# Kernel optimization log

Hardware: AMD Instinct MI355X
Metric: run time of the kernel (lower is better)

## Reference

```python
import jax, jax.numpy as jnp
import numpy as np

D = 512      # model_size
NH = 8       # num_heads
HD = D // NH # head_dim = 64
T = 2048     # seq len (qlen == klen == pos len)
B = 2        # batch

# flattened Bayesian parameter layout (matches flatten_list order in the module)
_SHAPES = [(3 * D, D), (D, D), (D, D), (3 * D,), (D,), (D,), (NH, HD), (NH, HD)]
_N = sum(int(np.prod(s)) for s in _SHAPES)  # 1,314,304


def _unflatten(w):
    out, i = [], 0
    for s in _SHAPES:
        n = int(np.prod(s))
        out.append(w[i:i + n].reshape(s))
        i += n
    return out


def _rel_shift(x):
    # Transformer-XL relative shift: x is [qlen, klen, B, NH]
    q, k, b, n = x.shape
    x = jnp.pad(x, ((0, 0), (1, 0), (0, 0), (0, 0)))  # zero col at front of klen axis
    x = x.reshape(k + 1, q, b, n)[1:]
    return x.reshape(q, k, b, n)


def setup_inputs() -> dict:
    key = jax.random.key(0)
    k1, k2, k3, k4, k5 = jax.random.split(key, 5)
    inp = jax.random.normal(k1, (T, B, D), dtype=jnp.float32)
    pos = jax.random.normal(k2, (T, 1, D), dtype=jnp.float32)
    std = np.sqrt(2.0 / (D + D))
    mu = jax.random.normal(k3, (_N,), dtype=jnp.float32) * std
    rho = -5.0 + 0.1 * jax.random.normal(k4, (_N,), dtype=jnp.float32)
    eps = jax.random.normal(k5, (_N,), dtype=jnp.float32)
    attn_mask = jnp.triu(jnp.ones((T, T), dtype=bool), 1)  # True = masked (future)
    return {"input": inp, "pos": pos, "attn_mask": attn_mask,
            "mu": mu, "rho": rho, "eps": eps}


def reference(input, pos, attn_mask, mu, rho, eps):
    # Gaussian reparameterized weight sample: w = mu + softplus(rho) * eps
    w = mu + jax.nn.softplus(rho) * eps
    (in_w, out_w, pos_w, in_b, out_b, pos_b, r_w_bias, r_r_bias) = _unflatten(w)

    # input projection -> q, k, v : [T, B, NH, HD]
    qkv = input @ in_w.T + in_b                      # [T, B, 3D]
    q, k, v = jnp.split(qkv, 3, axis=-1)
    q = q.reshape(T, B, NH, HD)
    k = k.reshape(T, B, NH, HD)
    v = v.reshape(T, B, NH, HD)

    # relative position projection: [R, NH, HD]
    r = (pos[:, 0, :] @ pos_w.T + pos_b).reshape(-1, NH, HD)

    # content score (AC) and position score (BD) with rel-shift
    AC = jnp.einsum('ibnd,jbnd->ijbn', q + r_w_bias, k)
    BD = _rel_shift(jnp.einsum('ibnd,jnd->ijbn', q + r_r_bias, r))

    scale = np.float32(1.0 / np.sqrt(HD))
    score = (AC + BD) * scale                        # [T, T, B, NH]
    score = jnp.where(attn_mask[:, :, None, None],
                      jnp.finfo(score.dtype).min, score)
    probs = jax.nn.softmax(score, axis=1)

    attn_vec = jnp.einsum('ijbn,jbnd->ibnd', probs, v).reshape(T, B, D)
    return attn_vec @ out_w.T + out_b                # [T, B, D]
```

## Files before the change

kernel.cpp:

```cpp
#include <hip/hip_runtime.h>


typedef float f32x4 __attribute__((ext_vector_type(4)));
typedef short bf16x8 __attribute__((ext_vector_type(8)));

#define NW 1314304
#define OFF_INB  1310720
#define OFF_INW  0
#define OFF_OUTW 786432
#define OFF_POSW 1048576
#define BB_IN  0
#define BB_OUT 1536
#define BB_POS 2048
#define BB_RW  2560
#define BB_RR  3072

#define L2E 1.44269504088896340736f

__device__ __forceinline__ unsigned short f2bf(float x) {
  unsigned u = __builtin_bit_cast(unsigned, x);
  u += 0x7fffu + ((u >> 16) & 1u);
  return (unsigned short)(u >> 16);
}
__device__ __forceinline__ float bf2f(unsigned short s) {
  return __builtin_bit_cast(float, ((unsigned)s) << 16);
}
__device__ __forceinline__ unsigned pk2(float lo, float hi) {
  return (unsigned)f2bf(lo) | ((unsigned)f2bf(hi) << 16);
}

__global__ void prep_kernel(const float* __restrict__ mu, const float* __restrict__ rho,
                            const float* __restrict__ eps,
                            const float* __restrict__ input, const float* __restrict__ pos,
                            unsigned short* __restrict__ Wh, float* __restrict__ Bf,
                            unsigned short* __restrict__ inH, unsigned short* __restrict__ posH) {
  const int bx = blockIdx.x;
  if (bx < 1284) {
    int i = (bx * 256 + threadIdx.x) * 4;
    if (i < NW) {
      float4 m = *(const float4*)&mu[i];
      float4 r = *(const float4*)&rho[i];
      float4 e = *(const float4*)&eps[i];
      float w0 = m.x + ((r.x > 20.f) ? r.x : log1pf(expf(r.x))) * e.x;
      float w1 = m.y + ((r.y > 20.f) ? r.y : log1pf(expf(r.y))) * e.y;
      float w2 = m.z + ((r.z > 20.f) ? r.z : log1pf(expf(r.z))) * e.z;
      float w3 = m.w + ((r.w > 20.f) ? r.w : log1pf(expf(r.w))) * e.w;
      union { unsigned short s[4]; uint2 u; } p;
      p.s[0] = f2bf(w0); p.s[1] = f2bf(w1); p.s[2] = f2bf(w2); p.s[3] = f2bf(w3);
      *(uint2*)&Wh[i] = p.u;
      if (i >= OFF_INB) {
        float4 b; b.x = w0; b.y = w1; b.z = w2; b.w = w3;
        *(float4*)&Bf[i - OFF_INB] = b;
      }
    }
  } else if (bx < 3332) {
    int i = ((bx - 1284) * 256 + threadIdx.x) * 4;
    float4 v = *(const float4*)&input[i];
    union { unsigned short s[4]; uint2 u; } p;
    p.s[0] = f2bf(v.x); p.s[1] = f2bf(v.y); p.s[2] = f2bf(v.z); p.s[3] = f2bf(v.w);
    *(uint2*)&inH[i] = p.u;
  } else {
    int i = ((bx - 3332) * 256 + threadIdx.x) * 4;
    float4 v = *(const float4*)&pos[i];
    union { unsigned short s[4]; uint2 u; } p;
    p.s[0] = f2bf(v.x); p.s[1] = f2bf(v.y); p.s[2] = f2bf(v.z); p.s[3] = f2bf(v.w);
    *(uint2*)&posH[i] = p.u;
  }
}

__device__ __forceinline__ void gemm_loop(const unsigned short* __restrict__ A,
                                          const unsigned short* __restrict__ B,
                                          unsigned short* As, unsigned short* Bs,
                                          f32x4 (&acc)[4]) {
  const int tid = threadIdx.x;
  const int wv = tid >> 6, lane = tid & 63, g = lane >> 4, cc = lane & 15;
  const int row = tid >> 2, q4 = tid & 3;
  const unsigned short* Ap = A + (size_t)row * 512 + 16 * q4;
  const unsigned short* Bp = B + (size_t)row * 512 + 16 * q4;

  *(uint4*)&As[row * 72 + 16 * q4]     = *(const uint4*)Ap;
  *(uint4*)&As[row * 72 + 16 * q4 + 8] = *(const uint4*)(Ap + 8);
  *(uint4*)&Bs[row * 72 + 16 * q4]     = *(const uint4*)Bp;
  *(uint4*)&Bs[row * 72 + 16 * q4 + 8] = *(const uint4*)(Bp + 8);
  __syncthreads();

  for (int it = 0; it < 8; it++) {
    uint4 a0, a1, b0, b1;
    const bool pf = (it < 7);
    if (pf) {
      const unsigned short* An = Ap + 64 * (it + 1);
      const unsigned short* Bn = Bp + 64 * (it + 1);
      a0 = *(const uint4*)An; a1 = *(const uint4*)(An + 8);
      b0 = *(const uint4*)Bn; b1 = *(const uint4*)(Bn + 8);
    }
    __builtin_amdgcn_s_setprio(1);
#pragma unroll
    for (int ks = 0; ks < 2; ks++) {
      bf16x8 af = *(const bf16x8*)&As[(16 * wv + cc) * 72 + 32 * ks + 8 * g];
#pragma unroll
      for (int fn = 0; fn < 4; fn++) {
        bf16x8 bf = *(const bf16x8*)&Bs[(16 * fn + cc) * 72 + 32 * ks + 8 * g];
        acc[fn] = __builtin_amdgcn_mfma_f32_16x16x32_bf16(af, bf, acc[fn], 0, 0, 0);
      }
    }
    __builtin_amdgcn_s_setprio(0);
    __syncthreads();
    if (pf) {
      *(uint4*)&As[row * 72 + 16 * q4]     = a0;
      *(uint4*)&As[row * 72 + 16 * q4 + 8] = a1;
      *(uint4*)&Bs[row * 72 + 16 * q4]     = b0;
      *(uint4*)&Bs[row * 72 + 16 * q4 + 8] = b1;
    }
    __syncthreads();
  }
}

__global__ __launch_bounds__(256, 2)
void gemm01_kernel(const unsigned short* __restrict__ inH, const unsigned short* __restrict__ posH,
                   const unsigned short* __restrict__ Wh, const float* __restrict__ Bf,
                   unsigned short* __restrict__ qrw, unsigned short* __restrict__ qrr,
                   unsigned short* __restrict__ kbuf, unsigned short* __restrict__ vT,
                   unsigned short* __restrict__ rbuf) {
  __shared__ __align__(16) unsigned short As[64 * 72];
  __shared__ __align__(16) unsigned short Bs[64 * 72];
  const int bx = blockIdx.x;
  const int tid = threadIdx.x;
  const int wv = tid >> 6, lane = tid & 63, g = lane >> 4, cc = lane & 15;

  const bool isR = (bx >= 1536);
  int m0, n0;
  const unsigned short *A, *W;
  if (!isR) {
    m0 = (bx & 63) << 6; n0 = (bx >> 6) << 6;
    A = inH + (size_t)m0 * 512;  W = Wh + OFF_INW + (size_t)n0 * 512;
  } else {
    const int t = bx - 1536;
    m0 = (t & 31) << 6; n0 = (t >> 5) << 6;
    A = posH + (size_t)m0 * 512; W = Wh + OFF_POSW + (size_t)n0 * 512;
  }

  f32x4 acc[4];
#pragma unroll
  for (int i = 0; i < 4; i++) { acc[i][0] = 0.f; acc[i][1] = 0.f; acc[i][2] = 0.f; acc[i][3] = 0.f; }
  gemm_loop(A, W, As, Bs, acc);

  const int nh2 = (n0 >> 6) & 7;
  const int sec = isR ? 3 : (n0 >> 9);

  if (sec == 0) {
#pragma unroll
    for (int fn = 0; fn < 4; fn++) {
      const int col = n0 + 16 * fn + cc;
      const float b0 = Bf[BB_IN + col];
      const float brw = Bf[BB_RW + col], brr = Bf[BB_RR + col];
#pragma unroll
      for (int r = 0; r < 4; r++) {
        const int ml = 16 * wv + 4 * g + r;
        As[ml * 72 + 16 * fn + cc] = f2bf((acc[fn][r] + b0 + brw) * 0.125f);
        Bs[ml * 72 + 16 * fn + cc] = f2bf((acc[fn][r] + b0 + brr) * 0.125f);
      }
    }
    __syncthreads();
    const int t0 = m0 >> 1;
#pragma unroll
    for (int pass = 0; pass < 2; pass++) {
      const int ch = tid + pass * 256;
      const int bb2 = ch >> 8, tl = (ch >> 3) & 31, hc = ch & 7;
      const int ml = 2 * tl + bb2;
      uint4 v1 = *(const uint4*)&As[ml * 72 + 8 * hc];
      uint4 v2 = *(const uint4*)&Bs[ml * 72 + 8 * hc];
      const size_t dst = ((size_t)(bb2 * 8 + nh2) * 2048 + t0 + tl) * 64 + 8 * hc;
      *(uint4*)&qrw[dst] = v1;
      *(uint4*)&qrr[dst] = v2;
    }
  } else if (sec == 1) {
#pragma unroll
    for (int fn = 0; fn < 4; fn++) {
      const int col = n0 + 16 * fn + cc;
      const float b0 = Bf[BB_IN + col];
#pragma unroll
      for (int r = 0; r < 4; r++)
        As[(16 * wv + 4 * g + r) * 72 + 16 * fn + cc] = f2bf(acc[fn][r] + b0);
    }
    __syncthreads();
    const int t0 = m0 >> 1;
#pragma unroll
    for (int pass = 0; pass < 2; pass++) {
      const int ch = tid + pass * 256;
      const int bb2 = ch >> 8, tl = (ch >> 3) & 31, hc = ch & 7;
      const int ml = 2 * tl + bb2;
      uint4 v1 = *(const uint4*)&As[ml * 72 + 8 * hc];
      *(uint4*)&kbuf[((size_t)(bb2 * 8 + nh2) * 2048 + t0 + tl) * 64 + 8 * hc] = v1;
    }
  } else if (sec == 2) {
#pragma unroll
    for (int fn = 0; fn < 4; fn++) {
      const int col = n0 + 16 * fn + cc;
#pragma unroll
      for (int r = 0; r < 4; r++)
        As[(16 * wv + 4 * g + r) * 72 + 16 * fn + cc] = f2bf(acc[fn][r] + Bf[BB_IN + col]);
    }
    __syncthreads();
#pragma unroll
    for (int cpass = 0; cpass < 2; cpass++) {
      const int ch = tid + cpass * 256;
      const int ncol = ch >> 3, bb2 = (ch >> 2) & 1, jc = ch & 3;
      union { unsigned short s[8]; uint4 u; } pk;
#pragma unroll
      for (int jj = 0; jj < 8; jj++)
        pk.s[jj] = As[(2 * (8 * jc + jj) + bb2) * 72 + ncol];
      *(uint4*)&vT[((size_t)(bb2 * 8 + nh2) * 64 + ncol) * 2048 + (m0 >> 1) + 8 * jc] = pk.u;
    }
  } else {
#pragma unroll
    for (int fn = 0; fn < 4; fn++) {
      const int col = n0 + 16 * fn + cc;
      const float b0 = Bf[BB_POS + col];
#pragma unroll
      for (int r = 0; r < 4; r++)
        As[(16 * wv + 4 * g + r) * 72 + 16 * fn + cc] = f2bf(acc[fn][r] + b0);
    }
    __syncthreads();
#pragma unroll
    for (int pass = 0; pass < 2; pass++) {
      const int ch = tid + pass * 256;
      const int ml = ch >> 3, hc = ch & 7;
      uint4 v1 = *(const uint4*)&As[ml * 72 + 8 * hc];
      *(uint4*)&rbuf[((size_t)nh2 * 2048 + m0 + ml) * 64 + 8 * hc] = v1;
    }
  }
}

__global__ __launch_bounds__(256, 2)
void gemmO_kernel(const unsigned short* __restrict__ av, const unsigned short* __restrict__ W,
                  const float* __restrict__ Bf, float* __restrict__ outp) {
  __shared__ __align__(16) unsigned short As[64 * 72];
  __shared__ __align__(16) unsigned short Bs[64 * 72];
  const int bx = blockIdx.x;
  const int tid = threadIdx.x;
  const int wv = tid >> 6, lane = tid & 63, g = lane >> 4, cc = lane & 15;
  const int m0 = (bx & 63) << 6, n0 = (bx >> 6) << 6;

  f32x4 acc[4];
#pragma unroll
  for (int i = 0; i < 4; i++) { acc[i][0] = 0.f; acc[i][1] = 0.f; acc[i][2] = 0.f; acc[i][3] = 0.f; }
  gemm_loop(av + (size_t)m0 * 512, W + (size_t)n0 * 512, As, Bs, acc);

#pragma unroll
  for (int fn = 0; fn < 4; fn++) {
    const int col = n0 + 16 * fn + cc;
#pragma unroll
    for (int r = 0; r < 4; r++) {
      const int mrow = m0 + 16 * wv + 4 * g + r;
      outp[(size_t)mrow * 512 + col] = acc[fn][r] + Bf[BB_OUT + col];
    }
  }
}

__global__ __launch_bounds__(256, 3)
void attn_kernel(const unsigned short* __restrict__ qrw, const unsigned short* __restrict__ qrr,
                 const unsigned short* __restrict__ kb, const unsigned short* __restrict__ vt,
                 const unsigned short* __restrict__ rb, unsigned short* __restrict__ av,
                 unsigned short* __restrict__ pO, float* __restrict__ pStats)
{
  __shared__ __align__(16) unsigned short Ks[64 * 72];
  __shared__ __align__(16) unsigned short Vs[64 * 72];
  __shared__ __align__(16) unsigned short Rs[128 * 72];
  __shared__ __align__(16) unsigned short GPs[4 * 16 * 84];

  const int tid = threadIdx.x;
  const int wv = tid >> 6, lane = tid & 63, g = lane >> 4, cc = lane & 15;
  const int bx = (int)blockIdx.x;
  const int bn = bx & 15;
  const int sid = 79 - (bx >> 4);
  int qt, s, ns;
  if (sid < 8)       { qt = sid;                s = 0;           ns = 1; }
  else if (sid < 24) { qt = 8 + ((sid - 8) >> 1); s = (sid - 8) & 1; ns = 2; }
  else if (sid < 48) { const int t = sid - 24; const int q3 = t / 3; qt = 16 + q3; s = t - 3 * q3; ns = 3; }
  else               { const int t = sid - 48; qt = 24 + (t >> 2); s = t & 3; ns = 4; }
  const int kt0 = s * 8;
  const int kt1 = (kt0 + 8 < qt + 1) ? (kt0 + 8) : (qt + 1);

  const int nh = bn & 7, bb = bn >> 3;
  const int i0 = qt * 64;
  const int i0g = i0 + wv * 16;
  const int w0base = 1984 - i0;

  const size_t qko = (size_t)bn * 2048 * 64;
  const size_t ro = (size_t)nh * 2048 * 64;

  bf16x8 qw[2], qr[2];
#pragma unroll
  for (int ks = 0; ks < 2; ks++) {
    qw[ks] = *(const bf16x8*)&qrw[qko + (size_t)(i0g + cc) * 64 + 32 * ks + 8 * g];
    qr[ks] = *(const bf16x8*)&qrr[qko + (size_t)(i0g + cc) * 64 + 32 * ks + 8 * g];
  }

  float m_run = -3.0e38f, l_run = 0.f;
  f32x4 o[4];
#pragma unroll
  for (int i = 0; i < 4; i++) { o[i][0] = 0.f; o[i][1] = 0.f; o[i][2] = 0.f; o[i][3] = 0.f; }

  const int srow = tid >> 2, sq = tid & 3;
  const int rrow = tid >> 1, rhalf = tid & 1;
  unsigned short* Gw = &GPs[wv * 1344];
  const int rbase = 48 - 16 * wv;

  {
    const unsigned short* kp = &kb[qko + (size_t)(kt0 * 64 + srow) * 64 + 16 * sq];
    *(uint4*)&Ks[srow * 72 + 16 * sq]     = *(const uint4*)kp;
    *(uint4*)&Ks[srow * 72 + 16 * sq + 8] = *(const uint4*)(kp + 8);
    const unsigned short* vp = &vt[qko + (size_t)srow * 2048 + kt0 * 64 + 16 * sq];
    *(uint4*)&Vs[srow * 72 + 16 * sq]     = *(const uint4*)vp;
    *(uint4*)&Vs[srow * 72 + 16 * sq + 8] = *(const uint4*)(vp + 8);
    const int u0 = w0base + kt0 * 64 + rrow;
    const int uc0 = u0 > 2047 ? 2047 : u0;
    const unsigned short* rp = &rb[ro + (size_t)uc0 * 64 + 32 * rhalf];
    unsigned short* rd = &Rs[(u0 & 127) * 72 + 32 * rhalf];
    *(uint4*)rd        = *(const uint4*)rp;
    *(uint4*)(rd + 8)  = *(const uint4*)(rp + 8);
    *(uint4*)(rd + 16) = *(const uint4*)(rp + 16);
    *(uint4*)(rd + 24) = *(const uint4*)(rp + 24);
  }
  __syncthreads();

  for (int kt = kt0; kt < kt1; kt++) {
    const int j0 = kt * 64;
    const int w0k = w0base + j0;
    const bool pf = (kt + 1 < kt1);

    uint4 ka0, ka1, va0, va1, ra0, ra1;
    int rslot = 0;
    if (pf) {
      const unsigned short* kp = &kb[qko + (size_t)(j0 + 64 + srow) * 64 + 16 * sq];
      ka0 = *(const uint4*)kp; ka1 = *(const uint4*)(kp + 8);
      const unsigned short* vp = &vt[qko + (size_t)srow * 2048 + j0 + 64 + 16 * sq];
      va0 = *(const uint4*)vp; va1 = *(const uint4*)(vp + 8);
      const int unew = w0k + 128 + (tid >> 2);
      rslot = unew & 127;
      const int uc = unew > 2047 ? 2047 : unew;
      const unsigned short* rp = &rb[ro + (size_t)uc * 64 + 16 * sq];
      ra0 = *(const uint4*)rp; ra1 = *(const uint4*)(rp + 8);
    }

    f32x4 st[4];
#pragma unroll
    for (int i = 0; i < 4; i++) { st[i][0] = 0.f; st[i][1] = 0.f; st[i][2] = 0.f; st[i][3] = 0.f; }
    __builtin_amdgcn_s_setprio(1);
#pragma unroll
    for (int ks = 0; ks < 2; ks++) {
#pragma unroll
      for (int fm = 0; fm < 4; fm++) {
        bf16x8 ka = *(const bf16x8*)&Ks[(16 * fm + cc) * 72 + 32 * ks + 8 * g];
        st[fm] = __builtin_amdgcn_mfma_f32_16x16x32_bf16(ka, qw[ks], st[fm], 0, 0, 0);
      }
    }
    f32x4 gt[5];
#pragma unroll
    for (int i = 0; i < 5; i++) { gt[i][0] = 0.f; gt[i][1] = 0.f; gt[i][2] = 0.f; gt[i][3] = 0.f; }
    const int rr0 = w0k + rbase + cc;
#pragma unroll
    for (int ks = 0; ks < 2; ks++) {
#pragma unroll
      for (int fm = 0; fm < 5; fm++) {
        const int rrw = (rr0 + 16 * fm) & 127;
        bf16x8 ra = *(const bf16x8*)&Rs[rrw * 72 + 32 * ks + 8 * g];
        gt[fm] = __builtin_amdgcn_mfma_f32_16x16x32_bf16(ra, qr[ks], gt[fm], 0, 0, 0);
      }
    }
    __builtin_amdgcn_s_setprio(0);

#pragma unroll
    for (int fm = 0; fm < 5; fm++) {
      uint2 w;
      w.x = pk2(gt[fm][0], gt[fm][1]);
      w.y = pk2(gt[fm][2], gt[fm][3]);
      *(uint2*)&Gw[cc * 84 + 16 * fm + 4 * g] = w;
    }

    float p[4][4];
    float tm = -3.0e38f;
    const bool diag = (kt == qt);
    const int c00 = 15 - cc + 4 * g;
#pragma unroll
    for (int fm = 0; fm < 4; fm++) {
      const int c0 = c00 + 16 * fm;
      const int e0 = c0 & ~1;
      const unsigned short* gp = &Gw[cc * 84 + e0];
      unsigned d0 = *(const unsigned*)gp;
      unsigned d1 = *(const unsigned*)(gp + 2);
      unsigned d2 = *(const unsigned*)(gp + 4);
      unsigned lo01, lo23;
      if (c0 & 1) { lo01 = (d0 >> 16) | (d1 << 16); lo23 = (d1 >> 16) | (d2 << 16); }
      else        { lo01 = d0; lo23 = d1; }
      float bd0 = bf2f((unsigned short)(lo01 & 0xffffu));
      float bd1 = bf2f((unsigned short)(lo01 >> 16));
      float bd2 = bf2f((unsigned short)(lo23 & 0xffffu));
      float bd3 = bf2f((unsigned short)(lo23 >> 16));
      float sv0 = st[fm][0] + bd0;
      float sv1 = st[fm][1] + bd1;
      float sv2 = st[fm][2] + bd2;
      float sv3 = st[fm][3] + bd3;
      if (diag) {
        const int jj = 16 * fm + 4 * g;
        const int lim = cc + 16 * wv;
        if (jj + 0 > lim) sv0 = -3.0e38f;
        if (jj + 1 > lim) sv1 = -3.0e38f;
        if (jj + 2 > lim) sv2 = -3.0e38f;
        if (jj + 3 > lim) sv3 = -3.0e38f;
      }
      p[fm][0] = sv0; p[fm][1] = sv1; p[fm][2] = sv2; p[fm][3] = sv3;
      tm = fmaxf(tm, fmaxf(fmaxf(sv0, sv1), fmaxf(sv2, sv3)));
    }
    tm = fmaxf(tm, __shfl_xor(tm, 16));
    tm = fmaxf(tm, __shfl_xor(tm, 32));
    const float m_new = fmaxf(m_run, tm);
    const float sc = exp2f((m_run - m_new) * L2E);
    float ps = 0.f;
#pragma unroll
    for (int fm = 0; fm < 4; fm++)
#pragma unroll
      for (int r = 0; r < 4; r++) {
        float pv = exp2f((p[fm][r] - m_new) * L2E);
        p[fm][r] = pv;
        ps += pv;
      }
    ps += __shfl_xor(ps, 16);
    ps += __shfl_xor(ps, 32);
    l_run = l_run * sc + ps;
    m_run = m_new;

    float scr[4];
#pragma unroll
    for (int r = 0; r < 4; r++) scr[r] = __shfl(sc, 4 * g + r);
#pragma unroll
    for (int fn = 0; fn < 4; fn++)
#pragma unroll
      for (int r = 0; r < 4; r++) o[fn][r] *= scr[r];

#pragma unroll
    for (int fm = 0; fm < 4; fm++) {
      uint2 w;
      w.x = pk2(p[fm][0], p[fm][1]);
      w.y = pk2(p[fm][2], p[fm][3]);
      *(uint2*)&Gw[cc * 72 + 16 * fm + 4 * g] = w;
    }
    bf16x8 pa[2];
#pragma unroll
    for (int ks = 0; ks < 2; ks++)
      pa[ks] = *(const bf16x8*)&Gw[cc * 72 + 32 * ks + 8 * g];

    __builtin_amdgcn_s_setprio(1);
#pragma unroll
    for (int ks = 0; ks < 2; ks++) {
#pragma unroll
      for (int fn = 0; fn < 4; fn++) {
        bf16x8 vb = *(const bf16x8*)&Vs[(16 * fn + cc) * 72 + 32 * ks + 8 * g];
        o[fn] = __builtin_amdgcn_mfma_f32_16x16x32_bf16(pa[ks], vb, o[fn], 0, 0, 0);
      }
    }
    __builtin_amdgcn_s_setprio(0);

    __syncthreads();
    if (pf) {
      *(uint4*)&Ks[srow * 72 + 16 * sq]     = ka0;
      *(uint4*)&Ks[srow * 72 + 16 * sq + 8] = ka1;
      *(uint4*)&Vs[srow * 72 + 16 * sq]     = va0;
      *(uint4*)&Vs[srow * 72 + 16 * sq + 8] = va1;
      unsigned short* rd = &Rs[rslot * 72 + 16 * sq];
      *(uint4*)rd       = ra0;
      *(uint4*)(rd + 8) = ra1;
    }
    __syncthreads();
  }

  if (ns == 1) {
    const float inv = 1.0f / l_run;
    float invr[4];
#pragma unroll
    for (int r = 0; r < 4; r++) invr[r] = __shfl(inv, 4 * g + r);
#pragma unroll
    for (int fn = 0; fn < 4; fn++) {
      const int hd = 16 * fn + cc;
#pragma unroll
      for (int r = 0; r < 4; r++) {
        const int irow = i0g + 4 * g + r;
        av[((size_t)(irow * 2 + bb) * 8 + nh) * 64 + hd] = f2bf(o[fn][r] * invr[r]);
      }
    }
  } else {
    const size_t slot = (size_t)(bn * 80 + sid);
#pragma unroll
    for (int fn = 0; fn < 4; fn++) {
      const int hd = 16 * fn + cc;
#pragma unroll
      for (int r = 0; r < 4; r++)
        pO[slot * 4096 + (16 * wv + 4 * g + r) * 64 + hd] = f2bf(o[fn][r]);
    }
    if (g == 0) {
      pStats[slot * 128 + (16 * wv + cc) * 2]     = m_run;
      pStats[slot * 128 + (16 * wv + cc) * 2 + 1] = l_run;
    }
  }
}

__global__ __launch_bounds__(256)
void combine_kernel(const unsigned short* __restrict__ pO, const float* __restrict__ pStats,
                    unsigned short* __restrict__ av) {
  const int bxx = (int)blockIdx.x;
  const int bn = bxx & 15, qt = 8 + (bxx >> 4);
  const int nh = bn & 7, bb = bn >> 3;
  const int ns = (qt >> 3) + 1;
  const int sid0 = (qt < 16) ? (8 + (qt - 8) * 2)
                 : (qt < 24) ? (24 + (qt - 16) * 3)
                             : (48 + (qt - 24) * 4);
  const int tid = threadIdx.x;
  const int ql = tid >> 2, hq = tid & 3;
  const size_t sb = (size_t)(bn * 80 + sid0);

  float M = -3.0e38f;
  for (int i = 0; i < ns; i++)
    M = fmaxf(M, pStats[(sb + i) * 128 + ql * 2]);

  float L = 0.f;
  float accv[16];
#pragma unroll
  for (int j = 0; j < 16; j++) accv[j] = 0.f;
  for (int i = 0; i < ns; i++) {
    const float mi = pStats[(sb + i) * 128 + ql * 2];
    const float li = pStats[(sb + i) * 128 + ql * 2 + 1];
    const float w = exp2f((mi - M) * L2E);
    L += w * li;
    union { uint4 u; unsigned short s[8]; } c0, c1;
    const unsigned short* src = &pO[(sb + i) * 4096 + ql * 64 + 16 * hq];
    c0.u = *(const uint4*)src;
    c1.u = *(const uint4*)(src + 8);
#pragma unroll
    for (int j = 0; j < 8; j++) accv[j]     += w * bf2f(c0.s[j]);
#pragma unroll
    for (int j = 0; j < 8; j++) accv[8 + j] += w * bf2f(c1.s[j]);
  }
  const float inv = 1.0f / L;
  union { uint4 u; unsigned short s[8]; } o0, o1;
#pragma unroll
  for (int j = 0; j < 8; j++) o0.s[j] = f2bf(accv[j] * inv);
#pragma unroll
  for (int j = 0; j < 8; j++) o1.s[j] = f2bf(accv[8 + j] * inv);
  const int q = qt * 64 + ql;
  unsigned short* dst = &av[((size_t)(q * 2 + bb) * 8 + nh) * 64 + 16 * hq];
  *(uint4*)dst       = o0.u;
  *(uint4*)(dst + 8) = o1.u;
}

extern "C" void kernel_launch(void* const* d_in, const int* in_sizes, int n_in,
                              void* d_out, int out_size, void* d_ws, size_t ws_size,
                              hipStream_t stream) {
  const float* input = (const float*)d_in[0];
  const float* pos   = (const float*)d_in[1];
  const float* mu  = (const float*)d_in[3];
  const float* rho = (const float*)d_in[4];
  const float* eps = (const float*)d_in[5];
  float* out = (float*)d_out;

  char* ws = (char*)d_ws;
  unsigned short* Wh   = (unsigned short*)ws;
  float*          Bf   = (float*)(ws + 2628608);
  unsigned short* inH  = (unsigned short*)(ws + 2642944);
  unsigned short* posH = (unsigned short*)(ws + 6837248);
  unsigned short* qrw  = (unsigned short*)(ws + 8934400);
  unsigned short* qrr  = (unsigned short*)(ws + 13128704);
  unsigned short* kbuf = (unsigned short*)(ws + 17323008);
  unsigned short* vT   = (unsigned short*)(ws + 21517312);
  unsigned short* rbuf = (unsigned short*)(ws + 25711616);
  unsigned short* pO   = (unsigned short*)(ws + 27808768);
  float*          pSt  = (float*)(ws + 38294528);
  unsigned short* av   = inH;

  prep_kernel<<<dim3(4356), dim3(256), 0, stream>>>(mu, rho, eps, input, pos, Wh, Bf, inH, posH);
  gemm01_kernel<<<dim3(1792), dim3(256), 0, stream>>>(inH, posH, Wh, Bf, qrw, qrr, kbuf, vT, rbuf);
  attn_kernel<<<dim3(1280), dim3(256), 0, stream>>>(qrw, qrr, kbuf, vT, rbuf, av, pO, pSt);
  combine_kernel<<<dim3(384), dim3(256), 0, stream>>>(pO, pSt, av);
  gemmO_kernel<<<dim3(512), dim3(256), 0, stream>>>(av, Wh + OFF_OUTW, Bf, out);
}
```

Measured before the change: 171.5 us.

## Enlarge projection GEMM tiles to 128x128 and defer softmax rescaling in attention

Both projection GEMMs (QKV/pos and output) now use 128x128 block tiles with a 2x2 wave layout and 4x4 MFMA accumulators per wave. This raises operand reuse per LDS load and cuts the block count, but it also lowers grid parallelism (128 blocks for gemmO on a large GPU) and raises register pressure. Separately, the attention kernel skips the running-max update and the output rescale when every lane's tile max exceeds the current max by at most 8. That leaves exponentials up to e^8 in fp32, which stays numerically safe.

```diff
diff --git a/kernel.cpp b/kernel.cpp
--- a/kernel.cpp
+++ b/kernel.cpp
@@ -68,48 +68,61 @@
   }
 }
 
-__device__ __forceinline__ void gemm_loop(const unsigned short* __restrict__ A,
-                                          const unsigned short* __restrict__ B,
-                                          unsigned short* As, unsigned short* Bs,
-                                          f32x4 (&acc)[4]) {
+__device__ __forceinline__ void gemm128_loop(const unsigned short* __restrict__ A,
+                                             const unsigned short* __restrict__ B,
+                                             unsigned short* As, unsigned short* Bs,
+                                             f32x4 (&acc)[4][4]) {
   const int tid = threadIdx.x;
   const int wv = tid >> 6, lane = tid & 63, g = lane >> 4, cc = lane & 15;
-  const int row = tid >> 2, q4 = tid & 3;
-  const unsigned short* Ap = A + (size_t)row * 512 + 16 * q4;
-  const unsigned short* Bp = B + (size_t)row * 512 + 16 * q4;
-
-  *(uint4*)&As[row * 72 + 16 * q4]     = *(const uint4*)Ap;
-  *(uint4*)&As[row * 72 + 16 * q4 + 8] = *(const uint4*)(Ap + 8);
-  *(uint4*)&Bs[row * 72 + 16 * q4]     = *(const uint4*)Bp;
-  *(uint4*)&Bs[row * 72 + 16 * q4 + 8] = *(const uint4*)(Bp + 8);
+  const int wr = wv >> 1, wc = wv & 1;
+  const int row = tid >> 1, half = tid & 1;
+  const unsigned short* Ap = A + (size_t)row * 512 + 32 * half;
+  const unsigned short* Bp = B + (size_t)row * 512 + 32 * half;
+  const int lb = row * 72 + 32 * half;
+
+#pragma unroll
+  for (int j = 0; j < 4; j++) {
+    *(uint4*)&As[lb + 8 * j] = *(const uint4*)(Ap + 8 * j);
+    *(uint4*)&Bs[lb + 8 * j] = *(const uint4*)(Bp + 8 * j);
+  }
   __syncthreads();
 
   for (int it = 0; it < 8; it++) {
-    uint4 a0, a1, b0, b1;
+    uint4 pa[4], pb[4];
     const bool pf = (it < 7);
     if (pf) {
       const unsigned short* An = Ap + 64 * (it + 1);
       const unsigned short* Bn = Bp + 64 * (it + 1);
-      a0 = *(const uint4*)An; a1 = *(const uint4*)(An + 8);
-      b0 = *(const uint4*)Bn; b1 = *(const uint4*)(Bn + 8);
+#pragma unroll
+      for (int j = 0; j < 4; j++) {
+        pa[j] = *(const uint4*)(An + 8 * j);
+        pb[j] = *(const uint4*)(Bn + 8 * j);
+      }
     }
     __builtin_amdgcn_s_setprio(1);
 #pragma unroll
     for (int ks = 0; ks < 2; ks++) {
-      bf16x8 af = *(const bf16x8*)&As[(16 * wv + cc) * 72 + 32 * ks + 8 * g];
-#pragma unroll
-      for (int fn = 0; fn < 4; fn++) {
-        bf16x8 bf = *(const bf16x8*)&Bs[(16 * fn + cc) * 72 + 32 * ks + 8 * g];
-        acc[fn] = __builtin_amdgcn_mfma_f32_16x16x32_bf16(af, bf, acc[fn], 0, 0, 0);
-      }
+      bf16x8 af[4], bf[4];
+#pragma unroll
+      for (int fm = 0; fm < 4; fm++)
+        af[fm] = *(const bf16x8*)&As[(64 * wr + 16 * fm + cc) * 72 + 32 * ks + 8 * g];
+#pragma unroll
+      for (int fn = 0; fn < 4; fn++)
+        bf[fn] = *(const bf16x8*)&Bs[(64 * wc + 16 * fn + cc) * 72 + 32 * ks + 8 * g];
+#pragma unroll
+      for (int fm = 0; fm < 4; fm++)
+#pragma unroll
+        for (int fn = 0; fn < 4; fn++)
+          acc[fm][fn] = __builtin_amdgcn_mfma_f32_16x16x32_bf16(af[fm], bf[fn], acc[fm][fn], 0, 0, 0);
     }
     __builtin_amdgcn_s_setprio(0);
     __syncthreads();
     if (pf) {
-      *(uint4*)&As[row * 72 + 16 * q4]     = a0;
-      *(uint4*)&As[row * 72 + 16 * q4 + 8] = a1;
-      *(uint4*)&Bs[row * 72 + 16 * q4]     = b0;
-      *(uint4*)&Bs[row * 72 + 16 * q4 + 8] = b1;
+#pragma unroll
+      for (int j = 0; j < 4; j++) {
+        *(uint4*)&As[lb + 8 * j] = pa[j];
+        *(uint4*)&Bs[lb + 8 * j] = pb[j];
+      }
     }
     __syncthreads();
   }
@@ -121,112 +134,128 @@
                    unsigned short* __restrict__ qrw, unsigned short* __restrict__ qrr,
                    unsigned short* __restrict__ kbuf, unsigned short* __restrict__ vT,
                    unsigned short* __restrict__ rbuf) {
-  __shared__ __align__(16) unsigned short As[64 * 72];
-  __shared__ __align__(16) unsigned short Bs[64 * 72];
+  __shared__ __align__(16) unsigned short As[128 * 72];
+  __shared__ __align__(16) unsigned short Bs[128 * 72];
   const int bx = blockIdx.x;
   const int tid = threadIdx.x;
   const int wv = tid >> 6, lane = tid & 63, g = lane >> 4, cc = lane & 15;
-
-  const bool isR = (bx >= 1536);
+  const int wr = wv >> 1, wc = wv & 1;
+
+  const bool isR = (bx >= 384);
   int m0, n0;
   const unsigned short *A, *W;
   if (!isR) {
-    m0 = (bx & 63) << 6; n0 = (bx >> 6) << 6;
+    m0 = (bx & 31) << 7; n0 = (bx >> 5) << 7;
     A = inH + (size_t)m0 * 512;  W = Wh + OFF_INW + (size_t)n0 * 512;
   } else {
-    const int t = bx - 1536;
-    m0 = (t & 31) << 6; n0 = (t >> 5) << 6;
+    const int t = bx - 384;
+    m0 = (t & 15) << 7; n0 = (t >> 4) << 7;
     A = posH + (size_t)m0 * 512; W = Wh + OFF_POSW + (size_t)n0 * 512;
   }
 
-  f32x4 acc[4];
-#pragma unroll
-  for (int i = 0; i < 4; i++) { acc[i][0] = 0.f; acc[i][1] = 0.f; acc[i][2] = 0.f; acc[i][3] = 0.f; }
-  gemm_loop(A, W, As, Bs, acc);
-
-  const int nh2 = (n0 >> 6) & 7;
+  f32x4 acc[4][4];
+#pragma unroll
+  for (int i = 0; i < 4; i++)
+#pragma unroll
+    for (int j = 0; j < 4; j++) { acc[i][j][0] = 0.f; acc[i][j][1] = 0.f; acc[i][j][2] = 0.f; acc[i][j][3] = 0.f; }
+  gemm128_loop(A, W, As, Bs, acc);
+
   const int sec = isR ? 3 : (n0 >> 9);
-
-  if (sec == 0) {
-#pragma unroll
-    for (int fn = 0; fn < 4; fn++) {
-      const int col = n0 + 16 * fn + cc;
-      const float b0 = Bf[BB_IN + col];
-      const float brw = Bf[BB_RW + col], brr = Bf[BB_RR + col];
-#pragma unroll
-      for (int r = 0; r < 4; r++) {
-        const int ml = 16 * wv + 4 * g + r;
-        As[ml * 72 + 16 * fn + cc] = f2bf((acc[fn][r] + b0 + brw) * 0.125f);
-        Bs[ml * 72 + 16 * fn + cc] = f2bf((acc[fn][r] + b0 + brr) * 0.125f);
-      }
-    }
-    __syncthreads();
-    const int t0 = m0 >> 1;
-#pragma unroll
-    for (int pass = 0; pass < 2; pass++) {
-      const int ch = tid + pass * 256;
-      const int bb2 = ch >> 8, tl = (ch >> 3) & 31, hc = ch & 7;
-      const int ml = 2 * tl + bb2;
-      uint4 v1 = *(const uint4*)&As[ml * 72 + 8 * hc];
-      uint4 v2 = *(const uint4*)&Bs[ml * 72 + 8 * hc];
-      const size_t dst = ((size_t)(bb2 * 8 + nh2) * 2048 + t0 + tl) * 64 + 8 * hc;
-      *(uint4*)&qrw[dst] = v1;
-      *(uint4*)&qrr[dst] = v2;
-    }
-  } else if (sec == 1) {
-#pragma unroll
-    for (int fn = 0; fn < 4; fn++) {
-      const int col = n0 + 16 * fn + cc;
-      const float b0 = Bf[BB_IN + col];
-#pragma unroll
-      for (int r = 0; r < 4; r++)
-        As[(16 * wv + 4 * g + r) * 72 + 16 * fn + cc] = f2bf(acc[fn][r] + b0);
-    }
-    __syncthreads();
-    const int t0 = m0 >> 1;
-#pragma unroll
-    for (int pass = 0; pass < 2; pass++) {
-      const int ch = tid + pass * 256;
-      const int bb2 = ch >> 8, tl = (ch >> 3) & 31, hc = ch & 7;
-      const int ml = 2 * tl + bb2;
-      uint4 v1 = *(const uint4*)&As[ml * 72 + 8 * hc];
-      *(uint4*)&kbuf[((size_t)(bb2 * 8 + nh2) * 2048 + t0 + tl) * 64 + 8 * hc] = v1;
-    }
-  } else if (sec == 2) {
-#pragma unroll
-    for (int fn = 0; fn < 4; fn++) {
-      const int col = n0 + 16 * fn + cc;
-#pragma unroll
-      for (int r = 0; r < 4; r++)
-        As[(16 * wv + 4 * g + r) * 72 + 16 * fn + cc] = f2bf(acc[fn][r] + Bf[BB_IN + col]);
-    }
-    __syncthreads();
-#pragma unroll
-    for (int cpass = 0; cpass < 2; cpass++) {
-      const int ch = tid + cpass * 256;
-      const int ncol = ch >> 3, bb2 = (ch >> 2) & 1, jc = ch & 3;
-      union { unsigned short s[8]; uint4 u; } pk;
-#pragma unroll
-      for (int jj = 0; jj < 8; jj++)
-        pk.s[jj] = As[(2 * (8 * jc + jj) + bb2) * 72 + ncol];
-      *(uint4*)&vT[((size_t)(bb2 * 8 + nh2) * 64 + ncol) * 2048 + (m0 >> 1) + 8 * jc] = pk.u;
-    }
-  } else {
-#pragma unroll
-    for (int fn = 0; fn < 4; fn++) {
-      const int col = n0 + 16 * fn + cc;
-      const float b0 = Bf[BB_POS + col];
-#pragma unroll
-      for (int r = 0; r < 4; r++)
-        As[(16 * wv + 4 * g + r) * 72 + 16 * fn + cc] = f2bf(acc[fn][r] + b0);
-    }
-    __syncthreads();
-#pragma unroll
-    for (int pass = 0; pass < 2; pass++) {
-      const int ch = tid + pass * 256;
-      const int ml = ch >> 3, hc = ch & 7;
-      uint4 v1 = *(const uint4*)&As[ml * 72 + 8 * hc];
-      *(uint4*)&rbuf[((size_t)nh2 * 2048 + m0 + ml) * 64 + 8 * hc] = v1;
+  const int t0 = m0 >> 1;
+
+#pragma unroll
+  for (int h = 0; h < 2; h++) {
+    const int nh2 = ((n0 + 64 * h) >> 6) & 7;
+    if (sec == 0) {
+      if (wc == h) {
+#pragma unroll
+        for (int fn = 0; fn < 4; fn++) {
+          const int colg = n0 + 64 * h + 16 * fn + cc;
+          const float b0 = Bf[BB_IN + colg];
+          const float brw = Bf[BB_RW + colg], brr = Bf[BB_RR + colg];
+#pragma unroll
+          for (int fm = 0; fm < 4; fm++)
+#pragma unroll
+            for (int r = 0; r < 4; r++) {
+              const int ml = 64 * wr + 16 * fm + 4 * g + r;
+              As[ml * 72 + 16 * fn + cc] = f2bf((acc[fm][fn][r] + b0 + brw) * 0.125f);
+              Bs[ml * 72 + 16 * fn + cc] = f2bf((acc[fm][fn][r] + b0 + brr) * 0.125f);
+            }
+        }
+      }
+      __syncthreads();
+      for (int c = tid; c < 1024; c += 256) {
+        const int ml = c >> 3, hc = c & 7;
+        const int bb2 = ml & 1, tl = ml >> 1;
+        uint4 v1 = *(const uint4*)&As[ml * 72 + 8 * hc];
+        uint4 v2 = *(const uint4*)&Bs[ml * 72 + 8 * hc];
+        const size_t dst = ((size_t)(bb2 * 8 + nh2) * 2048 + t0 + tl) * 64 + 8 * hc;
+        *(uint4*)&qrw[dst] = v1;
+        *(uint4*)&qrr[dst] = v2;
+      }
+      __syncthreads();
+    } else if (sec == 1) {
+      if (wc == h) {
+#pragma unroll
+        for (int fn = 0; fn < 4; fn++) {
+          const float b0 = Bf[BB_IN + n0 + 64 * h + 16 * fn + cc];
+#pragma unroll
+          for (int fm = 0; fm < 4; fm++)
+#pragma unroll
+            for (int r = 0; r < 4; r++)
+              As[(64 * wr + 16 * fm + 4 * g + r) * 72 + 16 * fn + cc] = f2bf(acc[fm][fn][r] + b0);
+        }
+      }
+      __syncthreads();
+      for (int c = tid; c < 1024; c += 256) {
+        const int ml = c >> 3, hc = c & 7;
+        const int bb2 = ml & 1, tl = ml >> 1;
+        uint4 v1 = *(const uint4*)&As[ml * 72 + 8 * hc];
+        *(uint4*)&kbuf[((size_t)(bb2 * 8 + nh2) * 2048 + t0 + tl) * 64 + 8 * hc] = v1;
+      }
+      __syncthreads();
+    } else if (sec == 2) {
+      if (wc == h) {
+#pragma unroll
+        for (int fn = 0; fn < 4; fn++) {
+          const float b0 = Bf[BB_IN + n0 + 64 * h + 16 * fn + cc];
+#pragma unroll
+          for (int fm = 0; fm < 4; fm++)
+#pragma unroll
+            for (int r = 0; r < 4; r++)
+              As[(64 * wr + 16 * fm + 4 * g + r) * 72 + 16 * fn + cc] = f2bf(acc[fm][fn][r] + b0);
+        }
+      }
+      __syncthreads();
+      for (int c = tid; c < 1024; c += 256) {
+        const int ncol = c >> 4;
+        const int rem = c & 15, bb2 = rem >> 3, jc = rem & 7;
+        union { unsigned short s[8]; uint4 u; } pk;
+#pragma unroll
+        for (int jt = 0; jt < 8; jt++)
+          pk.s[jt] = As[(2 * (8 * jc + jt) + bb2) * 72 + ncol];
+        *(uint4*)&vT[((size_t)(bb2 * 8 + nh2) * 64 + ncol) * 2048 + t0 + 8 * jc] = pk.u;
+      }
+      __syncthreads();
+    } else {
+      if (wc == h) {
+#pragma unroll
+        for (int fn = 0; fn < 4; fn++) {
+          const float b0 = Bf[BB_POS + n0 + 64 * h + 16 * fn + cc];
+#pragma unroll
+          for (int fm = 0; fm < 4; fm++)
+#pragma unroll
+            for (int r = 0; r < 4; r++)
+              As[(64 * wr + 16 * fm + 4 * g + r) * 72 + 16 * fn + cc] = f2bf(acc[fm][fn][r] + b0);
+        }
+      }
+      __syncthreads();
+      for (int c = tid; c < 1024; c += 256) {
+        const int ml = c >> 3, hc = c & 7;
+        uint4 v1 = *(const uint4*)&As[ml * 72 + 8 * hc];
+        *(uint4*)&rbuf[((size_t)nh2 * 2048 + m0 + ml) * 64 + 8 * hc] = v1;
+      }
+      __syncthreads();
     }
   }
 }
@@ -234,26 +263,32 @@
 __global__ __launch_bounds__(256, 2)
 void gemmO_kernel(const unsigned short* __restrict__ av, const unsigned short* __restrict__ W,
                   const float* __restrict__ Bf, float* __restrict__ outp) {
-  __shared__ __align__(16) unsigned short As[64 * 72];
-  __shared__ __align__(16) unsigned short Bs[64 * 72];
+  __shared__ __align__(16) unsigned short As[128 * 72];
+  __shared__ __align__(16) unsigned short Bs[128 * 72];
   const int bx = blockIdx.x;
   const int tid = threadIdx.x;
   const int wv = tid >> 6, lane = tid & 63, g = lane >> 4, cc = lane & 15;
-  const int m0 = (bx & 63) << 6, n0 = (bx >> 6) << 6;
-
-  f32x4 acc[4];
-#pragma unroll
-  for (int i = 0; i < 4; i++) { acc[i][0] = 0.f; acc[i][1] = 0.f; acc[i][2] = 0.f; acc[i][3] = 0.f; }
-  gemm_loop(av + (size_t)m0 * 512, W + (size_t)n0 * 512, As, Bs, acc);
+  const int wr = wv >> 1, wc = wv & 1;
+  const int m0 = (bx & 31) << 7, n0 = (bx >> 5) << 7;
+
+  f32x4 acc[4][4];
+#pragma unroll
+  for (int i = 0; i < 4; i++)
+#pragma unroll
+    for (int j = 0; j < 4; j++) { acc[i][j][0] = 0.f; acc[i][j][1] = 0.f; acc[i][j][2] = 0.f; acc[i][j][3] = 0.f; }
+  gemm128_loop(av + (size_t)m0 * 512, W + (size_t)n0 * 512, As, Bs, acc);
 
 #pragma unroll
   for (int fn = 0; fn < 4; fn++) {
-    const int col = n0 + 16 * fn + cc;
-#pragma unroll
-    for (int r = 0; r < 4; r++) {
-      const int mrow = m0 + 16 * wv + 4 * g + r;
-      outp[(size_t)mrow * 512 + col] = acc[fn][r] + Bf[BB_OUT + col];
-    }
+    const int col = n0 + 64 * wc + 16 * fn + cc;
+    const float b0 = Bf[BB_OUT + col];
+#pragma unroll
+    for (int fm = 0; fm < 4; fm++)
+#pragma unroll
+      for (int r = 0; r < 4; r++) {
+        const int mrow = m0 + 64 * wr + 16 * fm + 4 * g + r;
+        outp[(size_t)mrow * 512 + col] = acc[fm][fn][r] + b0;
+      }
   }
 }
 
@@ -414,8 +449,10 @@
     }
     tm = fmaxf(tm, __shfl_xor(tm, 16));
     tm = fmaxf(tm, __shfl_xor(tm, 32));
-    const float m_new = fmaxf(m_run, tm);
-    const float sc = exp2f((m_run - m_new) * L2E);
+    const bool defer = __all(tm - m_run <= 8.0f);
+    const float m_new = defer ? m_run : fmaxf(m_run, tm);
+    float sc = 1.0f;
+    if (!defer) sc = exp2f((m_run - m_new) * L2E);
     float ps = 0.f;
 #pragma unroll
     for (int fm = 0; fm < 4; fm++)
@@ -430,13 +467,15 @@
     l_run = l_run * sc + ps;
     m_run = m_new;
 
-    float scr[4];
-#pragma unroll
-    for (int r = 0; r < 4; r++) scr[r] = __shfl(sc, 4 * g + r);
-#pragma unroll
-    for (int fn = 0; fn < 4; fn++)
-#pragma unroll
-      for (int r = 0; r < 4; r++) o[fn][r] *= scr[r];
+    if (!defer) {
+      float scr[4];
+#pragma unroll
+      for (int r = 0; r < 4; r++) scr[r] = __shfl(sc, 4 * g + r);
+#pragma unroll
+      for (int fn = 0; fn < 4; fn++)
+#pragma unroll
+        for (int r = 0; r < 4; r++) o[fn][r] *= scr[r];
+    }
 
 #pragma unroll
     for (int fm = 0; fm < 4; fm++) {
@@ -577,8 +616,8 @@
   unsigned short* av   = inH;
 
   prep_kernel<<<dim3(4356), dim3(256), 0, stream>>>(mu, rho, eps, input, pos, Wh, Bf, inH, posH);
-  gemm01_kernel<<<dim3(1792), dim3(256), 0, stream>>>(inH, posH, Wh, Bf, qrw, qrr, kbuf, vT, rbuf);
+  gemm01_kernel<<<dim3(448), dim3(256), 0, stream>>>(inH, posH, Wh, Bf, qrw, qrr, kbuf, vT, rbuf);
   attn_kernel<<<dim3(1280), dim3(256), 0, stream>>>(qrw, qrr, kbuf, vT, rbuf, av, pO, pSt);
   combine_kernel<<<dim3(384), dim3(256), 0, stream>>>(pO, pSt, av);
-  gemmO_kernel<<<dim3(512), dim3(256), 0, stream>>>(av, Wh + OFF_OUTW, Bf, out);
-}
+  gemmO_kernel<<<dim3(128), dim3(256), 0, stream>>>(av, Wh + OFF_OUTW, Bf, out);
+}
```

New measurement: 211.7 us. 1.23x slower.
